# Kernel optimization log

Hardware: AMD Instinct MI355X
Metric: run time of the kernel (lower is better)

The kernel has to match this reference:

```python
import jax, jax.numpy as jnp
import numpy as np

N = 30000   # total nodes
E = 240000  # edges
B = 64      # graphs / proteins
H = 10      # GATv2 heads
C = 78      # per-head out dim (= xd_features)
D = H * C   # 780
SEQ = 1000
EMB = 128
LH = 64     # LSTM hidden per direction


def _lstm_dir(xs, Wih, Whh, bih, bhh, reverse):
    # xs: [T, Bn, EMB]; PyTorch gate order i,f,g,o
    Bn = xs.shape[1]
    h0 = jnp.zeros((Bn, LH), xs.dtype)
    def step(carry, xt):
        h, c = carry
        z = xt @ Wih.T + h @ Whh.T + bih + bhh
        i, f, g, o = jnp.split(z, 4, axis=-1)
        c = jax.nn.sigmoid(f) * c + jax.nn.sigmoid(i) * jnp.tanh(g)
        h = jax.nn.sigmoid(o) * jnp.tanh(c)
        return (h, c), h
    _, hs = jax.lax.scan(step, (h0, h0), xs, reverse=reverse)
    return hs


def setup_inputs() -> dict:
    k = jax.random.key(0)
    nxt = lambda i: jax.random.fold_in(k, i)
    s = 0.05
    d = {}
    d['x'] = jax.random.normal(nxt(0), (N, C), jnp.float32)
    d['edge_index'] = jax.random.randint(nxt(1), (2, E), 0, N)
    d['batch'] = jnp.sort(jax.random.randint(nxt(2), (N,), 0, B))
    d['target'] = jax.random.randint(nxt(3), (B, SEQ), 0, 26)
    # GATv2Conv params (share_weights=False)
    d['Wl'] = jax.random.normal(nxt(4), (C, D), jnp.float32) * s
    d['Wr'] = jax.random.normal(nxt(5), (C, D), jnp.float32) * s
    d['att'] = jax.random.normal(nxt(6), (H, C), jnp.float32) * s
    d['gat_b'] = jnp.zeros((D,), jnp.float32)
    # GCNConv params
    d['gcn_w'] = jax.random.normal(nxt(7), (D, D), jnp.float32) * s
    d['gcn_b'] = jnp.zeros((D,), jnp.float32)
    # protein branch
    d['emb'] = jax.random.normal(nxt(8), (26, EMB), jnp.float32) * s
    for tag, base in (('f', 9), ('b', 13)):
        d['Wih_' + tag] = jax.random.normal(nxt(base), (4 * LH, EMB), jnp.float32) * s
        d['Whh_' + tag] = jax.random.normal(nxt(base + 1), (4 * LH, LH), jnp.float32) * s
        d['bih_' + tag] = jnp.zeros((4 * LH,), jnp.float32)
        d['bhh_' + tag] = jnp.zeros((4 * LH,), jnp.float32)
    d['conv_w'] = jax.random.normal(nxt(17), (32, SEQ, 8), jnp.float32) * s
    d['conv_b'] = jnp.zeros((32,), jnp.float32)
    d['fcp_w'] = jax.random.normal(nxt(18), (32 * 121, 128), jnp.float32) * s
    d['fcp_b'] = jnp.zeros((128,), jnp.float32)
    # combined MLP (actual concat dim = 2*780 + 128 = 1688)
    d['fc1_w'] = jax.random.normal(nxt(19), (1688, 1024), jnp.float32) * s
    d['fc1_b'] = jnp.zeros((1024,), jnp.float32)
    d['fc2_w'] = jax.random.normal(nxt(20), (1024, 512), jnp.float32) * s
    d['fc2_b'] = jnp.zeros((512,), jnp.float32)
    d['out_w'] = jax.random.normal(nxt(21), (512, 1), jnp.float32) * s
    d['out_b'] = jnp.zeros((1,), jnp.float32)
    return d


def reference(x, edge_index, batch, target, Wl, Wr, att, gat_b, gcn_w, gcn_b,
              emb, Wih_f, Whh_f, bih_f, bhh_f, Wih_b, Whh_b, bih_b, bhh_b,
              conv_w, conv_b, fcp_w, fcp_b, fc1_w, fc1_b, fc2_w, fc2_b,
              out_w, out_b):
    # ---- graph branch (eval mode: dropout off) ----
    loops = jnp.arange(N)
    src = jnp.concatenate([edge_index[0], loops])  # self loops (PyG default)
    dst = jnp.concatenate([edge_index[1], loops])

    # GATv2Conv
    xl = (x @ Wl).reshape(N, H, C)
    xr = (x @ Wr).reshape(N, H, C)
    e = jax.nn.leaky_relu(xl[src] + xr[dst], 0.2)       # [E+N, H, C]
    logit = jnp.einsum('ehc,hc->eh', e, att)            # [E+N, H]
    m = jax.ops.segment_max(logit, dst, num_segments=N)
    ex = jnp.exp(logit - m[dst])
    den = jax.ops.segment_sum(ex, dst, num_segments=N)
    alpha = ex / den[dst]
    h = jax.ops.segment_sum(alpha[:, :, None] * xl[src], dst, num_segments=N)
    h = jax.nn.elu(h.reshape(N, D) + gat_b)

    # GCNConv with symmetric normalization
    hw = h @ gcn_w
    deg = jax.ops.segment_sum(jnp.ones_like(src, jnp.float32), dst, num_segments=N)
    dinv = jnp.where(deg > 0, jax.lax.rsqrt(jnp.maximum(deg, 1e-12)), 0.0)
    norm = dinv[src] * dinv[dst]
    g = jax.ops.segment_sum(norm[:, None] * hw[src], dst, num_segments=N) + gcn_b
    g = jax.nn.relu(g)

    # global max + mean pooling per graph
    gmax = jax.ops.segment_max(g, batch, num_segments=B)
    cnt = jax.ops.segment_sum(jnp.ones((N,), jnp.float32), batch, num_segments=B)
    gmean = jax.ops.segment_sum(g, batch, num_segments=B) / jnp.maximum(cnt, 1.0)[:, None]
    graph_feat = jnp.concatenate([gmax, gmean], axis=1)  # [B, 1560]

    # ---- protein branch ----
    et = emb[target]                                     # [B, SEQ, EMB]
    # nn.LSTM default batch_first=False: time axis is axis 0 (=B), batch axis is SEQ
    hf = _lstm_dir(et, Wih_f, Whh_f, bih_f, bhh_f, reverse=False)
    hb = _lstm_dir(et, Wih_b, Whh_b, bih_b, bhh_b, reverse=True)
    hcat = jnp.concatenate([hf, hb], axis=-1)            # [B, SEQ, 128]
    conv = jax.lax.conv_general_dilated(hcat, conv_w, (1,), 'VALID',
                                        dimension_numbers=('NCH', 'OIH', 'NCH'))
    conv = conv + conv_b[None, :, None]                  # [B, 32, 121]
    prot = conv.reshape(B, 32 * 121) @ fcp_w + fcp_b     # [B, 128]

    # ---- combined head ----
    comb = jnp.concatenate([graph_feat, prot], axis=1)   # [B, 1688]
    h1 = jax.nn.relu(comb @ fc1_w + fc1_b)
    h2 = jax.nn.relu(h1 @ fc2_w + fc2_b)
    return h2 @ out_w + out_b                            # [B, 1]
```

## Files before the change

kernel.cpp:

```cpp
#include <hip/hip_runtime.h>
#include <hip/hip_bf16.h>
#include <math.h>

static constexpr int NN   = 30000;
static constexpr int EE   = 240000;
static constexpr int ET   = EE + NN;
static constexpr int BB   = 64;
static constexpr int HH   = 10;
static constexpr int CC   = 78;
static constexpr int CCP  = 80;
static constexpr int DD   = HH * CC;
static constexpr int DDP  = HH * CCP;
static constexpr int SEQ  = 1000;
static constexpr int EMB  = 128;
static constexpr int LH   = 64;
static constexpr int COMBD = 2 * DD + 128;
static constexpr int PCHUNK = 64;

typedef __attribute__((ext_vector_type(8))) short short8;
typedef __attribute__((ext_vector_type(4))) float f32x4;

__device__ __forceinline__ float bf2f(unsigned short u) {
    return __uint_as_float(((unsigned int)u) << 16);
}
__device__ __forceinline__ float bflo(unsigned int u) {
    return __uint_as_float(u << 16);
}
__device__ __forceinline__ float bfhi(unsigned int u) {
    return __uint_as_float(u & 0xffff0000u);
}
__device__ __forceinline__ unsigned int pack2bf(float x, float y) {
    __hip_bfloat16 bx = __float2bfloat16(x), by = __float2bfloat16(y);
    unsigned short ux = *reinterpret_cast<unsigned short*>(&bx);
    unsigned short uy = *reinterpret_cast<unsigned short*>(&by);
    return (unsigned int)ux | ((unsigned int)uy << 16);
}
__device__ __forceinline__ float fast_sigmoid(float x) {
    return __builtin_amdgcn_rcpf(1.f + __expf(-x));
}
__device__ __forceinline__ float fast_tanh(float x) {
    float e = __expf(2.f * x);
    return 1.f - 2.f * __builtin_amdgcn_rcpf(e + 1.f);
}

template <int OBF, int PADHEAD>
__global__ __launch_bounds__(256) void gemm_bf16_mfma(const __hip_bfloat16* __restrict__ A,
                                                      const __hip_bfloat16* __restrict__ Bt,
                                                      void* __restrict__ Cv,
                                                      int M, int N, int K, int ldc) {
    constexpr int LDS_S = 40;
    __shared__ unsigned short As[128 * LDS_S];
    __shared__ unsigned short Bs[128 * LDS_S];
    const int tid  = threadIdx.x;
    const int lane = tid & 63, wid = tid >> 6;
    const int wr = wid >> 1, wc = wid & 1;
    const int l15 = lane & 15, l4 = lane >> 4;
    int l = blockIdx.y * gridDim.x + blockIdx.x;
    {
        int nwg = gridDim.x * gridDim.y;
        int q = nwg >> 3, r = nwg & 7;
        int xcd = l & 7, idx = l >> 3;
        l = (xcd < r) ? (xcd * (q + 1) + idx) : (r * (q + 1) + (xcd - r) * q + idx);
    }
    const int bm = (l / gridDim.x) * 128;
    const int bn = (l % gridDim.x) * 128;
    const int tr = tid >> 2, tc = (tid & 3) * 8;

    const unsigned short* Au = (const unsigned short*)A;
    const unsigned short* Bu = (const unsigned short*)Bt;

    f32x4 acc[4][4];
#pragma unroll
    for (int m = 0; m < 4; ++m)
#pragma unroll
        for (int n = 0; n < 4; ++n) acc[m][n] = (f32x4){0.f, 0.f, 0.f, 0.f};

    for (int k0 = 0; k0 < K; k0 += 32) {
#pragma unroll
        for (int half = 0; half < 2; ++half) {
            int row = tr + half * 64;
            {
                int grow = bm + row;
                short8 sv;
                if (grow < M && k0 + tc + 8 <= K) {
                    const unsigned int* p = (const unsigned int*)(Au + (size_t)grow * K + k0 + tc);
#pragma unroll
                    for (int j = 0; j < 4; ++j) {
                        unsigned int u = p[j];
                        sv[2 * j]     = (short)(u & 0xffffu);
                        sv[2 * j + 1] = (short)(u >> 16);
                    }
                } else {
#pragma unroll
                    for (int j = 0; j < 8; ++j) {
                        int gk = k0 + tc + j;
                        sv[j] = (grow < M && gk < K) ? (short)Au[(size_t)grow * K + gk] : (short)0;
                    }
                }
                *reinterpret_cast<short8*>(&As[row * LDS_S + tc]) = sv;
            }
            {
                int grow = bn + row;
                short8 sv;
                if (grow < N && k0 + tc + 8 <= K) {
                    const unsigned int* p = (const unsigned int*)(Bu + (size_t)grow * K + k0 + tc);
#pragma unroll
                    for (int j = 0; j < 4; ++j) {
                        unsigned int u = p[j];
                        sv[2 * j]     = (short)(u & 0xffffu);
                        sv[2 * j + 1] = (short)(u >> 16);
                    }
                } else {
#pragma unroll
                    for (int j = 0; j < 8; ++j) {
                        int gk = k0 + tc + j;
                        sv[j] = (grow < N && gk < K) ? (short)Bu[(size_t)grow * K + gk] : (short)0;
                    }
                }
                *reinterpret_cast<short8*>(&Bs[row * LDS_S + tc]) = sv;
            }
        }
        __syncthreads();
        short8 a[4], b[4];
#pragma unroll
        for (int m = 0; m < 4; ++m)
            a[m] = *reinterpret_cast<const short8*>(&As[(wr * 64 + m * 16 + l15) * LDS_S + l4 * 8]);
#pragma unroll
        for (int n = 0; n < 4; ++n)
            b[n] = *reinterpret_cast<const short8*>(&Bs[(wc * 64 + n * 16 + l15) * LDS_S + l4 * 8]);
#pragma unroll
        for (int m = 0; m < 4; ++m)
#pragma unroll
            for (int n = 0; n < 4; ++n)
                acc[m][n] = __builtin_amdgcn_mfma_f32_16x16x32_bf16(a[m], b[n], acc[m][n], 0, 0, 0);
        __syncthreads();
    }
#pragma unroll
    for (int m = 0; m < 4; ++m)
#pragma unroll
        for (int n = 0; n < 4; ++n)
#pragma unroll
            for (int r = 0; r < 4; ++r) {
                int row = bm + wr * 64 + m * 16 + l4 * 4 + r;
                int col = bn + wc * 64 + n * 16 + l15;
                if (row < M && col < N) {
                    int pc = PADHEAD ? ((col / CC) * CCP + (col % CC)) : col;
                    if (OBF)
                        ((__hip_bfloat16*)Cv)[(size_t)row * ldc + pc] = __float2bfloat16(acc[m][n][r]);
                    else
                        ((float*)Cv)[(size_t)row * ldc + pc] = acc[m][n][r];
                }
            }
}

__global__ void f32_to_bf16(const float* __restrict__ in, __hip_bfloat16* __restrict__ out, int n) {
    int i = blockIdx.x * blockDim.x + threadIdx.x;
    if (i < n) out[i] = __float2bfloat16(in[i]);
}

__global__ void transpose_to_bf16(const float* __restrict__ in, __hip_bfloat16* __restrict__ out,
                                  int Kdim, int Ndim) {
    int idx = blockIdx.x * blockDim.x + threadIdx.x;
    if (idx >= Kdim * Ndim) return;
    int n = idx / Kdim, k = idx % Kdim;
    out[idx] = __float2bfloat16(in[(size_t)k * Ndim + n]);
}

__global__ void transpose_f32(const float* __restrict__ in, float* __restrict__ out,
                              int Kdim, int Ndim) {
    int idx = blockIdx.x * blockDim.x + threadIdx.x;
    if (idx >= Kdim * Ndim) return;
    int n = idx / Kdim, k = idx % Kdim;
    out[idx] = in[(size_t)k * Ndim + n];
}

__global__ void pad_att(const float* __restrict__ att, float* __restrict__ att_p) {
    int idx = blockIdx.x * blockDim.x + threadIdx.x;
    if (idx >= HH * CCP) return;
    int h = idx / CCP, c = idx % CCP;
    att_p[idx] = (c < CC) ? att[h * CC + c] : 0.f;
}

__global__ void zero_pads(unsigned int* __restrict__ a, unsigned int* __restrict__ b) {
    int idx = blockIdx.x * blockDim.x + threadIdx.x;
    if (idx >= NN * HH) return;
    int n = idx / HH, h = idx % HH;
    size_t p = ((size_t)n * DDP + h * CCP + CC) >> 1;
    a[p] = 0u;
    b[p] = 0u;
}

template <int ACT>
__global__ __launch_bounds__(256) void gemm_skinny(const float* __restrict__ A,
                                                   const float* __restrict__ Bt,
                                                   const float* __restrict__ bias,
                                                   float* __restrict__ C,
                                                   int M, int N, int K, int ldc) {
    int oidx = blockIdx.x * 4 + (threadIdx.x >> 6);
    int lane = threadIdx.x & 63;
    if (oidx >= M * N) return;
    int row = oidx / N, col = oidx % N;
    const float4* a = (const float4*)(A + (size_t)row * K);
    const float4* b = (const float4*)(Bt + (size_t)col * K);
    int K4 = K >> 2;
    float s = 0.f;
    for (int i = lane; i < K4; i += 64) {
        float4 x = a[i], y = b[i];
        s += x.x * y.x + x.y * y.y + x.z * y.z + x.w * y.w;
    }
#pragma unroll
    for (int off = 32; off; off >>= 1) s += __shfl_xor(s, off);
    if (lane == 0) {
        s += bias[col];
        if (ACT == 1) s = fmaxf(s, 0.f);
        C[(size_t)row * ldc + col] = s;
    }
}

__global__ void deg_count(const int* __restrict__ ei, int* __restrict__ deg) {
    int e = blockIdx.x * blockDim.x + threadIdx.x;
    if (e >= ET) return;
    int d = (e < EE) ? ei[EE + e] : (e - EE);
    atomicAdd(&deg[d], 1);
}

__global__ __launch_bounds__(1024) void scan_kernel(const int* __restrict__ deg,
                                                    int* __restrict__ offs) {
    __shared__ int lds[1024];
    int tid = threadIdx.x;
    const int chunk = (NN + 1023) / 1024;
    int base = tid * chunk;
    int s = 0;
    for (int i = 0; i < chunk; ++i) {
        int idx = base + i;
        if (idx < NN) s += deg[idx];
    }
    lds[tid] = s;
    __syncthreads();
    for (int d = 1; d < 1024; d <<= 1) {
        int v = (tid >= d) ? lds[tid - d] : 0;
        __syncthreads();
        lds[tid] += v;
        __syncthreads();
    }
    int run = (tid == 0) ? 0 : lds[tid - 1];
    for (int i = 0; i < chunk; ++i) {
        int idx = base + i;
        if (idx < NN) { offs[idx] = run; run += deg[idx]; }
    }
    if (tid == 1023) offs[NN] = lds[1023];
}

__global__ void csr_fill(const int* __restrict__ ei, const int* __restrict__ offs,
                         int* __restrict__ cursor, int* __restrict__ csr_src,
                         int* __restrict__ csr_dst) {
    int e = blockIdx.x * blockDim.x + threadIdx.x;
    if (e >= ET) return;
    int s = (e < EE) ? ei[e] : (e - EE);
    int d = (e < EE) ? ei[EE + e] : (e - EE);
    int pos = atomicAdd(&cursor[d], 1);
    int slot = offs[d] + pos;
    csr_src[slot] = s;
    csr_dst[slot] = d;
}

__global__ void dinv_kernel(const int* __restrict__ deg, float* __restrict__ dinv) {
    int n = blockIdx.x * blockDim.x + threadIdx.x;
    if (n >= NN) return;
    float dg = (float)deg[n];
    dinv[n] = (dg > 0.f) ? 1.f / sqrtf(dg) : 0.f;
}

__device__ __forceinline__ float dot2lr(unsigned int a, unsigned int b, float w0, float w1) {
    float v0 = bflo(a) + bflo(b);
    float v1 = bfhi(a) + bfhi(b);
    v0 = (v0 > 0.f) ? v0 : 0.2f * v0;
    v1 = (v1 > 0.f) ? v1 : 0.2f * v1;
    return w0 * v0 + w1 * v1;
}

__global__ void gat_logits(const unsigned short* __restrict__ xl,
                           const unsigned short* __restrict__ xr,
                           const float* __restrict__ att_p, const int* __restrict__ csr_src,
                           const int* __restrict__ csr_dst, float* __restrict__ logit) {
    int idx = blockIdx.x * blockDim.x + threadIdx.x;
    if (idx >= ET * HH) return;
    int i = idx / HH, h = idx % HH;
    int s = csr_src[i], d = csr_dst[i];
    const uint4* pl = (const uint4*)(xl + (size_t)s * DDP + h * CCP);
    const uint4* pr = (const uint4*)(xr + (size_t)d * DDP + h * CCP);
    const float* pa = att_p + h * CCP;
    float acc = 0.f;
#pragma unroll
    for (int q = 0; q < CCP / 8; ++q) {
        uint4 a = pl[q], b = pr[q];
        const float* p8 = pa + q * 8;
        acc += dot2lr(a.x, b.x, p8[0], p8[1]);
        acc += dot2lr(a.y, b.y, p8[2], p8[3]);
        acc += dot2lr(a.z, b.z, p8[4], p8[5]);
        acc += dot2lr(a.w, b.w, p8[6], p8[7]);
    }
    logit[idx] = acc;
}

__global__ void gat_softmax(const int* __restrict__ offs, float* __restrict__ logit) {
    int idx = blockIdx.x * blockDim.x + threadIdx.x;
    if (idx >= NN * HH) return;
    int n = idx / HH, h = idx % HH;
    int i0 = offs[n], i1 = offs[n + 1];
    float m = -1e30f;
    for (int i = i0; i < i1; ++i) m = fmaxf(m, logit[i * HH + h]);
    float den = 0.f;
    for (int i = i0; i < i1; ++i) {
        float e = __expf(logit[i * HH + h] - m);
        logit[i * HH + h] = e;
        den += e;
    }
    float inv = __builtin_amdgcn_rcpf(den);
    for (int i = i0; i < i1; ++i) logit[i * HH + h] *= inv;
}

__global__ __launch_bounds__(256) void gat_aggregate(const int* __restrict__ offs,
                                                     const int* __restrict__ csr_src,
                                                     const float* __restrict__ alpha,
                                                     const unsigned int* __restrict__ xl,
                                                     const float* __restrict__ gat_b,
                                                     unsigned int* __restrict__ hout) {
    int n = blockIdx.x;
    int tid = threadIdx.x;
    int i0 = offs[n], i1 = offs[n + 1];
    const int U = DDP / 2;
    int u0 = tid, u1 = tid + 256;
    bool v1 = (u1 < U);
    int h0 = u0 / (CCP / 2), h1 = v1 ? u1 / (CCP / 2) : 0;
    float lo0 = 0.f, hi0 = 0.f, lo1 = 0.f, hi1 = 0.f;
    for (int i = i0; i < i1; ++i) {
        const unsigned int* row = xl + (size_t)csr_src[i] * U;
        const float* al = alpha + (size_t)i * HH;
        unsigned int w0 = row[u0];
        float p0 = al[h0];
        lo0 += p0 * bflo(w0);
        hi0 += p0 * bfhi(w0);
        if (v1) {
            unsigned int w1 = row[u1];
            float p1 = al[h1];
            lo1 += p1 * bflo(w1);
            hi1 += p1 * bfhi(w1);
        }
    }
    int m0 = u0 % (CCP / 2);
    if (m0 != (CCP / 2 - 1)) {
        int d = h0 * CC + 2 * m0;
        float x = lo0 + gat_b[d];     x = (x > 0.f) ? x : __expf(x) - 1.f;
        float y = hi0 + gat_b[d + 1]; y = (y > 0.f) ? y : __expf(y) - 1.f;
        hout[((size_t)n * DD + d) >> 1] = pack2bf(x, y);
    }
    if (v1) {
        int m1 = u1 % (CCP / 2);
        if (m1 != (CCP / 2 - 1)) {
            int d = h1 * CC + 2 * m1;
            float x = lo1 + gat_b[d];     x = (x > 0.f) ? x : __expf(x) - 1.f;
            float y = hi1 + gat_b[d + 1]; y = (y > 0.f) ? y : __expf(y) - 1.f;
            hout[((size_t)n * DD + d) >> 1] = pack2bf(x, y);
        }
    }
}

__global__ __launch_bounds__(256) void gcn_aggregate(const int* __restrict__ offs,
                                                     const int* __restrict__ csr_src,
                                                     const float* __restrict__ dinv,
                                                     const unsigned int* __restrict__ hw,
                                                     const float* __restrict__ gcn_b,
                                                     unsigned int* __restrict__ g) {
    int n = blockIdx.x;
    int tid = threadIdx.x;
    float din = dinv[n];
    int i0 = offs[n], i1 = offs[n + 1];
    const int U = DDP / 2;
    int u0 = tid, u1 = tid + 256;
    bool v1 = (u1 < U);
    float lo0 = 0.f, hi0 = 0.f, lo1 = 0.f, hi1 = 0.f;
    for (int i = i0; i < i1; ++i) {
        int s = csr_src[i];
        float w = dinv[s] * din;
        const unsigned int* row = hw + (size_t)s * U;
        unsigned int w0 = row[u0];
        lo0 += w * bflo(w0);
        hi0 += w * bfhi(w0);
        if (v1) {
            unsigned int w1 = row[u1];
            lo1 += w * bflo(w1);
            hi1 += w * bfhi(w1);
        }
    }
    int m0 = u0 % (CCP / 2);
    if (m0 != (CCP / 2 - 1)) {
        int d = (u0 / (CCP / 2)) * CC + 2 * m0;
        float x = fmaxf(lo0 + gcn_b[d], 0.f);
        float y = fmaxf(hi0 + gcn_b[d + 1], 0.f);
        g[(size_t)n * U + u0] = pack2bf(x, y);
    }
    if (v1) {
        int m1 = u1 % (CCP / 2);
        if (m1 != (CCP / 2 - 1)) {
            int d = (u1 / (CCP / 2)) * CC + 2 * m1;
            float x = fmaxf(lo1 + gcn_b[d], 0.f);
            float y = fmaxf(hi1 + gcn_b[d + 1], 0.f);
            g[(size_t)n * U + u1] = pack2bf(x, y);
        }
    }
}

__global__ void graph_ranges(const int* __restrict__ batch, int* __restrict__ gstart,
                             int* __restrict__ gend) {
    int n = blockIdx.x * blockDim.x + threadIdx.x;
    if (n >= NN) return;
    int b = batch[n];
    if (n == 0 || batch[n - 1] != b) gstart[b] = n;
    if (n == NN - 1 || batch[n + 1] != b) gend[b] = n + 1;
}

__global__ __launch_bounds__(256) void pool_partial(const unsigned int* __restrict__ g,
                                                    const int* __restrict__ batch,
                                                    float* __restrict__ pmax,
                                                    float* __restrict__ psum) {
    int chunk0 = blockIdx.x * PCHUNK;
    int tid = threadIdx.x;
    __shared__ int bsh[PCHUNK];
    for (int i = tid; i < PCHUNK; i += 256) {
        int n = chunk0 + i;
        bsh[i] = (n < NN) ? batch[n] : -1;
    }
    __syncthreads();
    const int U = DDP / 2;
    int u0 = tid, u1 = tid + 256;
    bool v1 = (u1 < U);
    float mA = 0.f, mB = 0.f, mC = 0.f, mD = 0.f;
    float sA = 0.f, sB = 0.f, sC = 0.f, sD = 0.f;
    int curb = bsh[0];
    auto flush = [&](int b) {
        if (b >= 0) {
            int m0 = u0 % (CCP / 2);
            if (m0 != (CCP / 2 - 1)) {
                int d = (u0 / (CCP / 2)) * CC + 2 * m0;
                atomicMax((unsigned int*)&pmax[(size_t)b * DD + d], __float_as_uint(mA));
                atomicAdd(&psum[(size_t)b * DD + d], sA);
                atomicMax((unsigned int*)&pmax[(size_t)b * DD + d + 1], __float_as_uint(mB));
                atomicAdd(&psum[(size_t)b * DD + d + 1], sB);
            }
            if (v1) {
                int m1 = u1 % (CCP / 2);
                if (m1 != (CCP / 2 - 1)) {
                    int d = (u1 / (CCP / 2)) * CC + 2 * m1;
                    atomicMax((unsigned int*)&pmax[(size_t)b * DD + d], __float_as_uint(mC));
                    atomicAdd(&psum[(size_t)b * DD + d], sC);
                    atomicMax((unsigned int*)&pmax[(size_t)b * DD + d + 1], __float_as_uint(mD));
                    atomicAdd(&psum[(size_t)b * DD + d + 1], sD);
                }
            }
        }
        mA = mB = mC = mD = 0.f;
        sA = sB = sC = sD = 0.f;
    };
    for (int i = 0; i < PCHUNK; ++i) {
        int n = chunk0 + i;
        if (n >= NN) break;
        int b = bsh[i];
        if (b != curb) { flush(curb); curb = b; }
        const unsigned int* row = g + (size_t)n * U;
        unsigned int w0 = row[u0];
        float x = bflo(w0), y = bfhi(w0);
        mA = fmaxf(mA, x); sA += x;
        mB = fmaxf(mB, y); sB += y;
        if (v1) {
            unsigned int w1 = row[u1];
            float z = bflo(w1), t = bfhi(w1);
            mC = fmaxf(mC, z); sC += z;
            mD = fmaxf(mD, t); sD += t;
        }
    }
    flush(curb);
}

__global__ void pool_finalize(const float* __restrict__ pmax, const float* __restrict__ psum,
                              const int* __restrict__ gstart, const int* __restrict__ gend,
                              float* __restrict__ comb) {
    int idx = blockIdx.x * blockDim.x + threadIdx.x;
    if (idx >= BB * DD) return;
    int b = idx / DD, d = idx % DD;
    float cnt = fmaxf((float)(gend[b] - gstart[b]), 1.f);
    comb[(size_t)b * COMBD + d] = pmax[idx];
    comb[(size_t)b * COMBD + DD + d] = psum[idx] / cnt;
}

__global__ void proj26_kernel(const float* __restrict__ emb,
                              const float* __restrict__ Wih_f, const float* __restrict__ bih_f,
                              const float* __restrict__ bhh_f,
                              const float* __restrict__ Wih_b, const float* __restrict__ bih_b,
                              const float* __restrict__ bhh_b, float* __restrict__ proj) {
    int dir = blockIdx.x, row = blockIdx.y, j = threadIdx.x;
    const float* W = dir ? Wih_b : Wih_f;
    const float* b1 = dir ? bih_b : bih_f;
    const float* b2 = dir ? bhh_b : bhh_f;
    float acc = b1[j] + b2[j];
    const float* e = emb + row * EMB;
    const float* w = W + j * EMB;
    for (int k = 0; k < EMB; ++k) acc += e[k] * w[k];
    proj[(dir * 26 + row) * 256 + j] = acc;
}

__global__ __launch_bounds__(256) void lstm_kernel(const int* __restrict__ target,
                                                   const float* __restrict__ proj26,
                                                   const float* __restrict__ Whh_f,
                                                   const float* __restrict__ Whh_b,
                                                   float* __restrict__ hcat) {
    int n = blockIdx.x;
    int dir = blockIdx.y;
    int tid = threadIdx.x;
    const float* Whh = dir ? Whh_b : Whh_f;
    const float* proj = proj26 + dir * 26 * 256;
    const int gate = tid >> 6;
    float w[LH];
#pragma unroll
    for (int u4 = 0; u4 < LH / 4; ++u4) {
        float4 v = *reinterpret_cast<const float4*>(Whh + tid * LH + u4 * 4);
        w[u4 * 4 + 0] = v.x; w[u4 * 4 + 1] = v.y;
        w[u4 * 4 + 2] = v.z; w[u4 * 4 + 3] = v.w;
    }
    __shared__ float h_lds[LH];
    __shared__ float z_lds[256];
    float c_reg = 0.f;
    if (tid < LH) h_lds[tid] = 0.f;
    __syncthreads();
    for (int s = 0; s < BB; ++s) {
        int t = dir ? (BB - 1 - s) : s;
        int tgt = target[t * SEQ + n];
        float a0 = 0.f, a1 = 0.f, a2 = 0.f, a3 = 0.f;
#pragma unroll
        for (int u = 0; u < LH; u += 4) {
            a0 += w[u] * h_lds[u];
            a1 += w[u + 1] * h_lds[u + 1];
            a2 += w[u + 2] * h_lds[u + 2];
            a3 += w[u + 3] * h_lds[u + 3];
        }
        float z = proj[tgt * 256 + tid] + a0 + a1 + a2 + a3;
        z_lds[tid] = (gate == 2) ? fast_tanh(z) : fast_sigmoid(z);
        __syncthreads();
        if (tid < LH) {
            float ig = z_lds[tid];
            float fg = z_lds[LH + tid];
            float gg = z_lds[2 * LH + tid];
            float og = z_lds[3 * LH + tid];
            float c = fg * c_reg + ig * gg;
            float h = og * fast_tanh(c);
            c_reg = c;
            h_lds[tid] = h;
            hcat[((size_t)t * SEQ + n) * 128 + dir * LH + tid] = h;
        }
        __syncthreads();
    }
}

__global__ __launch_bounds__(256) void transpose_hcat(const float* __restrict__ hcat,
                                                      unsigned short* __restrict__ hcatT) {
    int b = blockIdx.z;
    int i0 = blockIdx.y * 32;
    int h0 = blockIdx.x * 32;
    int th = threadIdx.x & 31;
    int ti = threadIdx.x >> 5;
    __shared__ float t[32][33];
#pragma unroll
    for (int r = 0; r < 4; ++r) {
        int i = i0 + ti + r * 8;
        if (i < SEQ) t[ti + r * 8][th] = hcat[((size_t)b * SEQ + i) * 128 + h0 + th];
    }
    __syncthreads();
#pragma unroll
    for (int r = 0; r < 4; ++r) {
        int h = h0 + ti + r * 8;
        int i = i0 + th;
        if (i < SEQ) {
            unsigned int u = __float_as_uint(t[th][ti + r * 8]);
            unsigned int lsb = (u >> 16) & 1u;
            u += 0x7fffu + lsb;
            hcatT[((size_t)b * 128 + h) * SEQ + i] = (unsigned short)(u >> 16);
        }
    }
}

__global__ void reshape_convw(const float* __restrict__ conv_w, __hip_bfloat16* __restrict__ wT) {
    int idx = blockIdx.x * blockDim.x + threadIdx.x;
    if (idx >= 256 * SEQ) return;
    int np = idx / SEQ, i = idx % SEQ;
    int o = np >> 3, k = np & 7;
    wT[idx] = __float2bfloat16(conv_w[((size_t)o * SEQ + i) * 8 + k]);
}

__global__ void conv_finalize(const float* __restrict__ T, const float* __restrict__ conv_b,
                              float* __restrict__ convout) {
    int idx = blockIdx.x * blockDim.x + threadIdx.x;
    if (idx >= BB * 32 * 121) return;
    int p = idx % 121;
    int o = (idx / 121) % 32;
    int b = idx / (121 * 32);
    float acc = conv_b[o];
#pragma unroll
    for (int k = 0; k < 8; ++k)
        acc += T[(size_t)(b * 128 + p + k) * 256 + o * 8 + k];
    convout[(size_t)b * 3872 + o * 121 + p] = acc;
}

extern "C" void kernel_launch(void* const* d_in, const int* in_sizes, int n_in,
                              void* d_out, int out_size, void* d_ws, size_t ws_size,
                              hipStream_t stream) {
    const float* x      = (const float*)d_in[0];
    const int*   ei     = (const int*)d_in[1];
    const int*   batch  = (const int*)d_in[2];
    const int*   target = (const int*)d_in[3];
    const float* Wl     = (const float*)d_in[4];
    const float* Wr     = (const float*)d_in[5];
    const float* att    = (const float*)d_in[6];
    const float* gat_b  = (const float*)d_in[7];
    const float* gcn_w  = (const float*)d_in[8];
    const float* gcn_b  = (const float*)d_in[9];
    const float* emb    = (const float*)d_in[10];
    const float* Wih_f  = (const float*)d_in[11];
    const float* Whh_f  = (const float*)d_in[12];
    const float* bih_f  = (const float*)d_in[13];
    const float* bhh_f  = (const float*)d_in[14];
    const float* Wih_b  = (const float*)d_in[15];
    const float* Whh_b  = (const float*)d_in[16];
    const float* bih_b  = (const float*)d_in[17];
    const float* bhh_b  = (const float*)d_in[18];
    const float* conv_w = (const float*)d_in[19];
    const float* conv_b = (const float*)d_in[20];
    const float* fcp_w  = (const float*)d_in[21];
    const float* fcp_b  = (const float*)d_in[22];
    const float* fc1_w  = (const float*)d_in[23];
    const float* fc1_b  = (const float*)d_in[24];
    const float* fc2_w  = (const float*)d_in[25];
    const float* fc2_b  = (const float*)d_in[26];
    const float* out_w  = (const float*)d_in[27];
    const float* out_b  = (const float*)d_in[28];
    float* out = (float*)d_out;
    (void)n_in; (void)in_sizes; (void)out_size;

    char* ws = (char*)d_ws;
    size_t o = 0;
    auto alloc = [&](size_t bytes) {
        char* p = ws + o;
        o = (o + bytes + 255) & ~(size_t)255;
        return p;
    };
    constexpr size_t HALF = (size_t)NN * DDP * 2;
    char* region = (char*)alloc(2 * HALF);
    __hip_bfloat16* xl_bf = (__hip_bfloat16*)region;
    __hip_bfloat16* xr_bf = (__hip_bfloat16*)(region + HALF);
    __hip_bfloat16* hw_bf = (__hip_bfloat16*)region;
    __hip_bfloat16* g_bf  = (__hip_bfloat16*)(region + HALF);
    char* rp = region;
    auto palloc = [&](size_t bytes) {
        char* p = rp;
        rp += (bytes + 255) & ~(size_t)255;
        return p;
    };
    float* hcat    = (float*)palloc((size_t)BB * SEQ * 128 * 4);
    float* proj26  = (float*)palloc(2 * 26 * 256 * 4);
    float* convout = (float*)palloc((size_t)BB * 3872 * 4);
    __hip_bfloat16* wT = (__hip_bfloat16*)palloc((size_t)256 * SEQ * 2);
    unsigned short* hcatT = (unsigned short*)palloc((size_t)BB * 128 * SEQ * 2);
    float* T = (float*)palloc((size_t)BB * 128 * 256 * 4);
    __hip_bfloat16* h_bf  = (__hip_bfloat16*)alloc((size_t)NN * DD * 2);
    __hip_bfloat16* x_bf  = (__hip_bfloat16*)alloc((size_t)NN * CC * 2);
    __hip_bfloat16* wl_t  = (__hip_bfloat16*)alloc((size_t)DD * CC * 2);
    __hip_bfloat16* wr_t  = (__hip_bfloat16*)alloc((size_t)DD * CC * 2);
    __hip_bfloat16* gcw_t = (__hip_bfloat16*)alloc((size_t)DD * DD * 2);
    float* att_p  = (float*)alloc((size_t)HH * CCP * 4);
    float* fcp_wt = (float*)alloc((size_t)3872 * 128 * 4);
    float* fc1_wt = (float*)alloc((size_t)COMBD * 1024 * 4);
    float* fc2_wt = (float*)alloc((size_t)1024 * 512 * 4);
    float* out_wt = (float*)alloc((size_t)512 * 4);
    float* logit    = (float*)alloc((size_t)ET * HH * 4);
    int*   csr_src  = (int*)alloc((size_t)ET * 4);
    int*   csr_dst  = (int*)alloc((size_t)ET * 4);
    int*   deg      = (int*)alloc((size_t)NN * 4);
    int*   cursor   = (int*)alloc((size_t)NN * 4);
    int*   offs     = (int*)alloc((size_t)(NN + 1) * 4);
    float* dinv     = (float*)alloc((size_t)NN * 4);
    int*   gstart   = (int*)alloc(64 * 4);
    int*   gend     = (int*)alloc(64 * 4);
    float* pmax     = (float*)alloc((size_t)BB * DD * 4);
    float* psum     = (float*)alloc((size_t)BB * DD * 4);
    float* comb     = (float*)alloc((size_t)BB * COMBD * 4);
    float* h1       = (float*)alloc((size_t)BB * 1024 * 4);
    float* h2       = (float*)alloc((size_t)BB * 512 * 4);
    if (o > ws_size) return;

    hipMemsetAsync(deg, 0, (size_t)NN * 4, stream);
    hipMemsetAsync(cursor, 0, (size_t)NN * 4, stream);
    hipMemsetAsync(gstart, 0, 64 * 4, stream);
    hipMemsetAsync(gend, 0, 64 * 4, stream);
    hipMemsetAsync(pmax, 0, (size_t)BB * DD * 4, stream);
    hipMemsetAsync(psum, 0, (size_t)BB * DD * 4, stream);

    {
        dim3 grid(2, 26);
        proj26_kernel<<<grid, 256, 0, stream>>>(emb, Wih_f, bih_f, bhh_f, Wih_b, bih_b, bhh_b, proj26);
    }
    {
        dim3 grid(SEQ, 2);
        lstm_kernel<<<grid, 256, 0, stream>>>(target, proj26, Whh_f, Whh_b, hcat);
    }
    {
        dim3 grid(4, 32, BB);
        transpose_hcat<<<grid, 256, 0, stream>>>(hcat, hcatT);
    }
    reshape_convw<<<(256 * SEQ + 255) / 256, 256, 0, stream>>>(conv_w, wT);
    {
        dim3 grid(2, 64);
        gemm_bf16_mfma<0, 0><<<grid, 256, 0, stream>>>((const __hip_bfloat16*)hcatT, wT, T,
                                                       BB * 128, 256, SEQ, 256);
    }
    conv_finalize<<<(BB * 32 * 121 + 255) / 256, 256, 0, stream>>>(T, conv_b, convout);
    transpose_f32<<<(3872 * 128 + 255) / 256, 256, 0, stream>>>(fcp_w, fcp_wt, 3872, 128);
    gemm_skinny<0><<<(BB * 128 + 3) / 4, 256, 0, stream>>>(convout, fcp_wt, fcp_b,
                                                           comb + 2 * DD, BB, 128, 3872, COMBD);

    f32_to_bf16<<<(NN * CC + 255) / 256, 256, 0, stream>>>(x, x_bf, NN * CC);
    transpose_to_bf16<<<(CC * DD + 255) / 256, 256, 0, stream>>>(Wl, wl_t, CC, DD);
    transpose_to_bf16<<<(CC * DD + 255) / 256, 256, 0, stream>>>(Wr, wr_t, CC, DD);
    transpose_to_bf16<<<(DD * DD + 255) / 256, 256, 0, stream>>>(gcn_w, gcw_t, DD, DD);
    pad_att<<<(HH * CCP + 255) / 256, 256, 0, stream>>>(att, att_p);
    transpose_f32<<<(COMBD * 1024 + 255) / 256, 256, 0, stream>>>(fc1_w, fc1_wt, COMBD, 1024);
    transpose_f32<<<(1024 * 512 + 255) / 256, 256, 0, stream>>>(fc2_w, fc2_wt, 1024, 512);
    transpose_f32<<<(512 + 255) / 256, 256, 0, stream>>>(out_w, out_wt, 512, 1);

    dim3 ggrid((DD + 127) / 128, (NN + 127) / 128);
    gemm_bf16_mfma<1, 1><<<ggrid, 256, 0, stream>>>(x_bf, wl_t, xl_bf, NN, DD, CC, DDP);
    gemm_bf16_mfma<1, 1><<<ggrid, 256, 0, stream>>>(x_bf, wr_t, xr_bf, NN, DD, CC, DDP);
    zero_pads<<<(NN * HH + 255) / 256, 256, 0, stream>>>((unsigned int*)xl_bf, (unsigned int*)xr_bf);
    deg_count<<<(ET + 255) / 256, 256, 0, stream>>>(ei, deg);
    scan_kernel<<<1, 1024, 0, stream>>>(deg, offs);
    csr_fill<<<(ET + 255) / 256, 256, 0, stream>>>(ei, offs, cursor, csr_src, csr_dst);
    dinv_kernel<<<(NN + 255) / 256, 256, 0, stream>>>(deg, dinv);
    gat_logits<<<(ET * HH + 255) / 256, 256, 0, stream>>>((const unsigned short*)xl_bf,
                                                          (const unsigned short*)xr_bf,
                                                          att_p, csr_src, csr_dst, logit);
    gat_softmax<<<(NN * HH + 255) / 256, 256, 0, stream>>>(offs, logit);
    gat_aggregate<<<NN, 256, 0, stream>>>(offs, csr_src, logit,
                                          (const unsigned int*)xl_bf, gat_b,
                                          (unsigned int*)h_bf);
    gemm_bf16_mfma<1, 1><<<ggrid, 256, 0, stream>>>(h_bf, gcw_t, hw_bf, NN, DD, DD, DDP);
    gcn_aggregate<<<NN, 256, 0, stream>>>(offs, csr_src, dinv,
                                          (const unsigned int*)hw_bf, gcn_b,
                                          (unsigned int*)g_bf);
    graph_ranges<<<(NN + 255) / 256, 256, 0, stream>>>(batch, gstart, gend);
    pool_partial<<<(NN + PCHUNK - 1) / PCHUNK, 256, 0, stream>>>((const unsigned int*)g_bf,
                                                                 batch, pmax, psum);
    pool_finalize<<<(BB * DD + 255) / 256, 256, 0, stream>>>(pmax, psum, gstart, gend, comb);

    gemm_skinny<1><<<(BB * 1024 + 3) / 4, 256, 0, stream>>>(comb, fc1_wt, fc1_b, h1,
                                                            BB, 1024, COMBD, 1024);
    gemm_skinny<1><<<(BB * 512 + 3) / 4, 256, 0, stream>>>(h1, fc2_wt, fc2_b, h2,
                                                           BB, 512, 1024, 512);
    gemm_skinny<0><<<(BB + 3) / 4, 256, 0, stream>>>(h2, out_wt, out_b, out,
                                                     BB, 1, 512, 1);
}
```

Baseline: 941.8 us.

## Use direct global-to-LDS loads in node GEMMs with padded operand layouts

Adds a new bf16 MFMA GEMM that loads A and B tiles straight into shared memory via global_load_lds, with no bounds checks. To make that safe, x, the GAT weights, the GCN weight and the GAT output are zero-padded to tile-aligned shapes, and the GCN weight is remapped to the head-padded K layout. The GAT aggregate now writes the padded 800-wide layout directly, so the GCN GEMM consumes it without repacking. This aims to cut register staging and bounds-check overhead in the three large node GEMMs, at the cost of a single-buffered loop with no prefetch, extra padded K work, and larger buffers.

```diff
diff --git a/kernel.cpp b/kernel.cpp
--- a/kernel.cpp
+++ b/kernel.cpp
@@ -11,6 +11,9 @@
 static constexpr int CCP  = 80;
 static constexpr int DD   = HH * CC;
 static constexpr int DDP  = HH * CCP;
+static constexpr int NNP  = 30080;
+static constexpr int KXP  = 96;
+static constexpr int NBP  = 896;
 static constexpr int SEQ  = 1000;
 static constexpr int EMB  = 128;
 static constexpr int LH   = 64;
@@ -41,6 +44,78 @@
 __device__ __forceinline__ float fast_tanh(float x) {
     float e = __expf(2.f * x);
     return 1.f - 2.f * __builtin_amdgcn_rcpf(e + 1.f);
+}
+__device__ __forceinline__ void glds16(const unsigned short* g, unsigned short* l) {
+    __builtin_amdgcn_global_load_lds(
+        (const __attribute__((address_space(1))) unsigned int*)g,
+        (__attribute__((address_space(3))) unsigned int*)l, 16, 0, 0);
+}
+
+template <int PADHEAD>
+__global__ __launch_bounds__(256) void gemm_glds(const __hip_bfloat16* __restrict__ A,
+                                                 const __hip_bfloat16* __restrict__ Bt,
+                                                 __hip_bfloat16* __restrict__ C,
+                                                 int M, int N, int Kp, int ldc) {
+    __shared__ unsigned short As[128 * 32];
+    __shared__ unsigned short Bs[128 * 32];
+    const int tid  = threadIdx.x;
+    const int lane = tid & 63, wid = tid >> 6;
+    const int wr = wid >> 1, wc = wid & 1;
+    const int l15 = lane & 15, l4 = lane >> 4;
+    int l = blockIdx.y * gridDim.x + blockIdx.x;
+    {
+        int nwg = gridDim.x * gridDim.y;
+        int q = nwg >> 3, r = nwg & 7;
+        int xcd = l & 7, idx = l >> 3;
+        l = (xcd < r) ? (xcd * (q + 1) + idx) : (r * (q + 1) + (xcd - r) * q + idx);
+    }
+    const int bm = (l / gridDim.x) * 128;
+    const int bn = (l % gridDim.x) * 128;
+    const unsigned short* Au = (const unsigned short*)A;
+    const unsigned short* Bu = (const unsigned short*)Bt;
+    const int lrow = lane >> 2, lseg = (lane & 3) * 8;
+
+    f32x4 acc[4][4];
+#pragma unroll
+    for (int m = 0; m < 4; ++m)
+#pragma unroll
+        for (int n = 0; n < 4; ++n) acc[m][n] = (f32x4){0.f, 0.f, 0.f, 0.f};
+
+    for (int k0 = 0; k0 < Kp; k0 += 32) {
+#pragma unroll
+        for (int c = 0; c < 2; ++c) {
+            int rbase = wid * 32 + c * 16;
+            glds16(Au + (size_t)(bm + rbase + lrow) * Kp + k0 + lseg, &As[rbase * 32]);
+            glds16(Bu + (size_t)(bn + rbase + lrow) * Kp + k0 + lseg, &Bs[rbase * 32]);
+        }
+        __syncthreads();
+        short8 a[4], b[4];
+#pragma unroll
+        for (int m = 0; m < 4; ++m)
+            a[m] = *reinterpret_cast<const short8*>(&As[(wr * 64 + m * 16 + l15) * 32 + l4 * 8]);
+#pragma unroll
+        for (int n = 0; n < 4; ++n)
+            b[n] = *reinterpret_cast<const short8*>(&Bs[(wc * 64 + n * 16 + l15) * 32 + l4 * 8]);
+#pragma unroll
+        for (int m = 0; m < 4; ++m)
+#pragma unroll
+            for (int n = 0; n < 4; ++n)
+                acc[m][n] = __builtin_amdgcn_mfma_f32_16x16x32_bf16(a[m], b[n], acc[m][n], 0, 0, 0);
+        __syncthreads();
+    }
+#pragma unroll
+    for (int m = 0; m < 4; ++m)
+#pragma unroll
+        for (int n = 0; n < 4; ++n)
+#pragma unroll
+            for (int r = 0; r < 4; ++r) {
+                int row = bm + wr * 64 + m * 16 + l4 * 4 + r;
+                int col = bn + wc * 64 + n * 16 + l15;
+                if (row < M && col < N) {
+                    int pc = PADHEAD ? ((col / CC) * CCP + (col % CC)) : col;
+                    C[(size_t)row * ldc + pc] = __float2bfloat16(acc[m][n][r]);
+                }
+            }
 }
 
 template <int OBF, int PADHEAD>
@@ -153,17 +228,30 @@
             }
 }
 
-__global__ void f32_to_bf16(const float* __restrict__ in, __hip_bfloat16* __restrict__ out, int n) {
-    int i = blockIdx.x * blockDim.x + threadIdx.x;
-    if (i < n) out[i] = __float2bfloat16(in[i]);
-}
-
-__global__ void transpose_to_bf16(const float* __restrict__ in, __hip_bfloat16* __restrict__ out,
-                                  int Kdim, int Ndim) {
-    int idx = blockIdx.x * blockDim.x + threadIdx.x;
-    if (idx >= Kdim * Ndim) return;
-    int n = idx / Kdim, k = idx % Kdim;
-    out[idx] = __float2bfloat16(in[(size_t)k * Ndim + n]);
+__global__ void pad_x(const float* __restrict__ x, __hip_bfloat16* __restrict__ xp) {
+    int idx = blockIdx.x * blockDim.x + threadIdx.x;
+    if (idx >= NNP * KXP) return;
+    int r = idx / KXP, c = idx % KXP;
+    float v = (r < NN && c < CC) ? x[(size_t)r * CC + c] : 0.f;
+    xp[idx] = __float2bfloat16(v);
+}
+
+__global__ void pad_wT(const float* __restrict__ w, __hip_bfloat16* __restrict__ wt) {
+    int idx = blockIdx.x * blockDim.x + threadIdx.x;
+    if (idx >= NBP * KXP) return;
+    int n = idx / KXP, k = idx % KXP;
+    float v = (n < DD && k < CC) ? w[(size_t)k * DD + n] : 0.f;
+    wt[idx] = __float2bfloat16(v);
+}
+
+__global__ void pad_gcwT(const float* __restrict__ w, __hip_bfloat16* __restrict__ wt) {
+    int idx = blockIdx.x * blockDim.x + threadIdx.x;
+    if (idx >= NBP * DDP) return;
+    int n = idx / DDP, kp = idx % DDP;
+    int kc = kp % CCP;
+    int k = (kp / CCP) * CC + kc;
+    float v = (n < DD && kc < CC) ? w[(size_t)k * DD + n] : 0.f;
+    wt[idx] = __float2bfloat16(v);
 }
 
 __global__ void transpose_f32(const float* __restrict__ in, float* __restrict__ out,
@@ -348,21 +436,24 @@
             hi1 += p1 * bfhi(w1);
         }
     }
+    unsigned int ov0 = 0u, ov1 = 0u;
     int m0 = u0 % (CCP / 2);
     if (m0 != (CCP / 2 - 1)) {
         int d = h0 * CC + 2 * m0;
         float x = lo0 + gat_b[d];     x = (x > 0.f) ? x : __expf(x) - 1.f;
         float y = hi0 + gat_b[d + 1]; y = (y > 0.f) ? y : __expf(y) - 1.f;
-        hout[((size_t)n * DD + d) >> 1] = pack2bf(x, y);
-    }
+        ov0 = pack2bf(x, y);
+    }
+    hout[(size_t)n * U + u0] = ov0;
     if (v1) {
         int m1 = u1 % (CCP / 2);
         if (m1 != (CCP / 2 - 1)) {
             int d = h1 * CC + 2 * m1;
             float x = lo1 + gat_b[d];     x = (x > 0.f) ? x : __expf(x) - 1.f;
             float y = hi1 + gat_b[d + 1]; y = (y > 0.f) ? y : __expf(y) - 1.f;
-            hout[((size_t)n * DD + d) >> 1] = pack2bf(x, y);
-        }
+            ov1 = pack2bf(x, y);
+        }
+        hout[(size_t)n * U + u1] = ov1;
     }
 }
 
@@ -670,11 +761,11 @@
     __hip_bfloat16* wT = (__hip_bfloat16*)palloc((size_t)256 * SEQ * 2);
     unsigned short* hcatT = (unsigned short*)palloc((size_t)BB * 128 * SEQ * 2);
     float* T = (float*)palloc((size_t)BB * 128 * 256 * 4);
-    __hip_bfloat16* h_bf  = (__hip_bfloat16*)alloc((size_t)NN * DD * 2);
-    __hip_bfloat16* x_bf  = (__hip_bfloat16*)alloc((size_t)NN * CC * 2);
-    __hip_bfloat16* wl_t  = (__hip_bfloat16*)alloc((size_t)DD * CC * 2);
-    __hip_bfloat16* wr_t  = (__hip_bfloat16*)alloc((size_t)DD * CC * 2);
-    __hip_bfloat16* gcw_t = (__hip_bfloat16*)alloc((size_t)DD * DD * 2);
+    __hip_bfloat16* h_bf  = (__hip_bfloat16*)alloc((size_t)NNP * DDP * 2);
+    __hip_bfloat16* x_bf  = (__hip_bfloat16*)alloc((size_t)NNP * KXP * 2);
+    __hip_bfloat16* wl_t  = (__hip_bfloat16*)alloc((size_t)NBP * KXP * 2);
+    __hip_bfloat16* wr_t  = (__hip_bfloat16*)alloc((size_t)NBP * KXP * 2);
+    __hip_bfloat16* gcw_t = (__hip_bfloat16*)alloc((size_t)NBP * DDP * 2);
     float* att_p  = (float*)alloc((size_t)HH * CCP * 4);
     float* fcp_wt = (float*)alloc((size_t)3872 * 128 * 4);
     float* fc1_wt = (float*)alloc((size_t)COMBD * 1024 * 4);
@@ -726,18 +817,18 @@
     gemm_skinny<0><<<(BB * 128 + 3) / 4, 256, 0, stream>>>(convout, fcp_wt, fcp_b,
                                                            comb + 2 * DD, BB, 128, 3872, COMBD);
 
-    f32_to_bf16<<<(NN * CC + 255) / 256, 256, 0, stream>>>(x, x_bf, NN * CC);
-    transpose_to_bf16<<<(CC * DD + 255) / 256, 256, 0, stream>>>(Wl, wl_t, CC, DD);
-    transpose_to_bf16<<<(CC * DD + 255) / 256, 256, 0, stream>>>(Wr, wr_t, CC, DD);
-    transpose_to_bf16<<<(DD * DD + 255) / 256, 256, 0, stream>>>(gcn_w, gcw_t, DD, DD);
+    pad_x<<<(NNP * KXP + 255) / 256, 256, 0, stream>>>(x, x_bf);
+    pad_wT<<<(NBP * KXP + 255) / 256, 256, 0, stream>>>(Wl, wl_t);
+    pad_wT<<<(NBP * KXP + 255) / 256, 256, 0, stream>>>(Wr, wr_t);
+    pad_gcwT<<<(NBP * DDP + 255) / 256, 256, 0, stream>>>(gcn_w, gcw_t);
     pad_att<<<(HH * CCP + 255) / 256, 256, 0, stream>>>(att, att_p);
     transpose_f32<<<(COMBD * 1024 + 255) / 256, 256, 0, stream>>>(fc1_w, fc1_wt, COMBD, 1024);
     transpose_f32<<<(1024 * 512 + 255) / 256, 256, 0, stream>>>(fc2_w, fc2_wt, 1024, 512);
     transpose_f32<<<(512 + 255) / 256, 256, 0, stream>>>(out_w, out_wt, 512, 1);
 
-    dim3 ggrid((DD + 127) / 128, (NN + 127) / 128);
-    gemm_bf16_mfma<1, 1><<<ggrid, 256, 0, stream>>>(x_bf, wl_t, xl_bf, NN, DD, CC, DDP);
-    gemm_bf16_mfma<1, 1><<<ggrid, 256, 0, stream>>>(x_bf, wr_t, xr_bf, NN, DD, CC, DDP);
+    dim3 ggrid((DD + 127) / 128, NNP / 128);
+    gemm_glds<1><<<ggrid, 256, 0, stream>>>(x_bf, wl_t, xl_bf, NN, DD, KXP, DDP);
+    gemm_glds<1><<<ggrid, 256, 0, stream>>>(x_bf, wr_t, xr_bf, NN, DD, KXP, DDP);
     zero_pads<<<(NN * HH + 255) / 256, 256, 0, stream>>>((unsigned int*)xl_bf, (unsigned int*)xr_bf);
     deg_count<<<(ET + 255) / 256, 256, 0, stream>>>(ei, deg);
     scan_kernel<<<1, 1024, 0, stream>>>(deg, offs);
@@ -750,7 +841,10 @@
     gat_aggregate<<<NN, 256, 0, stream>>>(offs, csr_src, logit,
                                           (const unsigned int*)xl_bf, gat_b,
                                           (unsigned int*)h_bf);
-    gemm_bf16_mfma<1, 1><<<ggrid, 256, 0, stream>>>(h_bf, gcw_t, hw_bf, NN, DD, DD, DDP);
+    {
+        dim3 g2((DD + 127) / 128, NNP / 128);
+        gemm_glds<1><<<g2, 256, 0, stream>>>(h_bf, gcw_t, hw_bf, NN, DD, DDP, DDP);
+    }
     gcn_aggregate<<<NN, 256, 0, stream>>>(offs, csr_src, dinv,
                                           (const unsigned int*)hw_bf, gcn_b,
                                           (unsigned int*)g_bf);
```

After: 870.9 us. 7.5% less time.
